# Optimization experiments

Hardware: AMD Instinct MI355X
Metric: run time of the kernel (lower is better)

## Reference

```python
import jax, jax.numpy as jnp
import numpy as np

V, B, T, D, F, E = 16000, 8, 1024, 64, 256, 8


def setup_inputs() -> dict:
    key = jax.random.key(0)
    ks = jax.random.split(key, 8)
    s = 0.02
    return {
        "x": jax.random.randint(ks[0], (B, T), 0, V),
        "embed_table": jax.random.normal(ks[1], (V, D), jnp.float32) * s,
        "Wm": jax.random.normal(ks[2], (D, D), jnp.float32) * s,
        "Um": jax.random.normal(ks[3], (D, D), jnp.float32) * s,
        "bm": jnp.zeros((D,), jnp.float32),
        "Wg": jax.random.normal(ks[4], (D, E), jnp.float32) * s,
        "bg": jnp.zeros((E,), jnp.float32),
        "W1": jax.random.normal(ks[5], (E, D, F), jnp.float32) * s,
        "b1": jnp.zeros((E, F), jnp.float32),
        "W2": jax.random.normal(ks[6], (E, F, D), jnp.float32) * s,
        "b2": jnp.zeros((E, D), jnp.float32),
        "ln_g": jnp.ones((D,), jnp.float32),
        "ln_b": jnp.zeros((D,), jnp.float32),
        "head_W": jax.random.normal(ks[7], (D, V), jnp.float32) * s,
        "head_b": jnp.zeros((V,), jnp.float32),
    }


def _layernorm(y, g, b, eps=1e-5):
    mu = jnp.mean(y, axis=-1, keepdims=True)
    var = jnp.mean((y - mu) ** 2, axis=-1, keepdims=True)
    return g * (y - mu) * jax.lax.rsqrt(var + eps) + b


def reference(x, embed_table, Wm, Um, bm, Wg, bg, W1, b1, W2, b2, ln_g, ln_b, head_W, head_b):
    emb = embed_table[x]                    # [B, T, D]
    emb_t = jnp.swapaxes(emb, 0, 1)         # [T, B, D] for scan over time

    def step(mem, x_t):
        # recurrent router: state update then gate computation
        mem_new = jnp.tanh(x_t @ Wm + mem @ Um + bm)              # [B, D]
        gates = jax.nn.softmax(mem_new @ Wg + bg, axis=-1)        # [B, E]
        # all-experts dense FFN (exact erf GELU as in torch default)
        h = jax.nn.gelu(jnp.einsum('bd,edf->bef', x_t, W1) + b1, approximate=False)
        eo = jnp.einsum('bef,efd->bed', h, W2) + b2               # [B, E, D]
        moe = jnp.einsum('be,bed->bd', gates, eo)                 # gated sum
        out_t = _layernorm(x_t + moe, ln_g, ln_b)
        return mem_new, out_t

    mem0 = jnp.zeros((x.shape[0], emb.shape[-1]), emb.dtype)
    _, outs = jax.lax.scan(step, mem0, emb_t)   # outs: [T, B, D]
    out = jnp.swapaxes(outs, 0, 1)              # [B, T, D]
    logits = out @ head_W + head_b              # [B, T, V]
    # training_mode=False -> no pred_loss branch; avg_pred_loss == 0.0
    return logits
```

## Files before the change

### kernel.cpp

```cpp
#include <hip/hip_runtime.h>


#define VV 16000
#define BB 8
#define TT 1024
#define DD 64
#define FF 256
#define EE 8
#define BT 8192

typedef unsigned short u16;
typedef unsigned int   u32;
typedef __attribute__((ext_vector_type(8))) short short8;
typedef __attribute__((ext_vector_type(4))) float f32x4;
typedef __attribute__((ext_vector_type(2))) float f32x2;

__device__ __forceinline__ float bf2f(u16 u) {
    union { u32 i; float f; } v; v.i = ((u32)u) << 16; return v.f;
}
__device__ __forceinline__ u16 f2bf(float f) {
    union { float f; u32 i; } v; v.f = f;
    u32 lsb = (v.i >> 16) & 1u;
    return (u16)((v.i + 0x7fffu + lsb) >> 16);
}
__device__ __forceinline__ short8 ld8(const u16* p) { return *(const short8*)p; }
__device__ __forceinline__ float ldf(const void* p, int i, int isbf) {
    return isbf ? bf2f(((const u16*)p)[i]) : ((const float*)p)[i];
}

__global__ __launch_bounds__(256) void k_sniff(const u32* __restrict__ tblw,
                                               int* __restrict__ flag) {
    __shared__ int c;
    int tid = threadIdx.x;
    if (tid == 0) c = 0;
    __syncthreads();
    u32 u = tblw[tid];
    u32 lo = u & 0xFFFFu;
    u32 e = (lo >> 7) & 0xFFu;
    int hit = ((e >= 0x60u && e <= 0x7Eu) || lo == 0u) ? 1 : 0;
    atomicAdd(&c, hit);
    __syncthreads();
    if (tid == 0) *flag = (c >= 192) ? 1 : 0;
}

__global__ __launch_bounds__(256) void k_transph(const void* __restrict__ headW,
                                                 const int* __restrict__ flag,
                                                 u16* __restrict__ headWT) {
    __shared__ float tile[DD][DD + 1];
    int isbf = *flag;
    int v0 = blockIdx.x * 64;
    int tid = threadIdx.x;
    int c = tid & 63, rq = tid >> 6;
#pragma unroll
    for (int i = 0; i < 16; i++) {
        int k = i * 4 + rq;
        tile[k][c] = ldf(headW, k * VV + v0 + c, isbf);
    }
    __syncthreads();
#pragma unroll
    for (int i = 0; i < 16; i++) {
        int v = i * 4 + rq;
        headWT[(v0 + v) * DD + c] = f2bf(tile[c][v]);
    }
}

__global__ __launch_bounds__(256) void k_transpose(const void* __restrict__ W1,
                                                   const void* __restrict__ W2,
                                                   const int* __restrict__ flag,
                                                   u16* __restrict__ W1T,
                                                   u16* __restrict__ W2T) {
    int isbf = *flag;
    int idx = blockIdx.x * 256 + threadIdx.x;
    if (idx < EE * DD * FF) {
        int e = idx >> 14, r = idx & 16383, d = r >> 8, f = r & 255;
        W1T[e * 16384 + f * DD + d] = f2bf(ldf(W1, idx, isbf));
    } else {
        int j2 = idx - EE * DD * FF;
        int e = j2 >> 14, r = j2 & 16383, f = r >> 6, d = r & 63;
        W2T[e * 16384 + d * FF + f] = f2bf(ldf(W2, j2, isbf));
    }
}

__global__ __launch_bounds__(256) void k_embed_pre(const int* __restrict__ x,
                                                   const void* __restrict__ tbl,
                                                   const void* __restrict__ Wm,
                                                   const void* __restrict__ bm,
                                                   const int* __restrict__ flag,
                                                   u16* __restrict__ emb,
                                                   float* __restrict__ pre) {
    __shared__ float sWm[DD * DD];
    __shared__ float sbm[DD];
    int isbf = *flag;
    int tid = threadIdx.x;
    for (int i = tid; i < DD * DD; i += 256) sWm[i] = ldf(Wm, i, isbf);
    if (tid < DD) sbm[tid] = ldf(bm, tid, isbf);
    __syncthreads();

    int gi = blockIdx.x * 256 + tid;
    int tok = gi >> 2, q = gi & 3;
    int id = x[tok];
    float e[DD];
    if (isbf) {
        const uint4* src = (const uint4*)((const u16*)tbl + id * DD);
        uint4* dst = (uint4*)(emb + tok * DD);
#pragma unroll
        for (int i = 0; i < 8; i++) {
            uint4 v = src[i];
            if ((i >> 1) == q) dst[i] = v;
            const u16* pu = (const u16*)&v;
#pragma unroll
            for (int j = 0; j < 8; j++) e[i * 8 + j] = bf2f(pu[j]);
        }
    } else {
        const float4* src = (const float4*)((const float*)tbl + id * DD);
        u16* dst = emb + tok * DD;
#pragma unroll
        for (int i = 0; i < 16; i++) {
            float4 v = src[i];
            e[i * 4 + 0] = v.x; e[i * 4 + 1] = v.y;
            e[i * 4 + 2] = v.z; e[i * 4 + 3] = v.w;
            if ((i >> 2) == q) {
                u32 p0 = (u32)f2bf(v.x) | ((u32)f2bf(v.y) << 16);
                u32 p1 = (u32)f2bf(v.z) | ((u32)f2bf(v.w) << 16);
                ((u32*)dst)[i * 2] = p0;
                ((u32*)dst)[i * 2 + 1] = p1;
            }
        }
    }
    int b = tok >> 10, t = tok & 1023;
    float* prow = pre + (t * BB + b) * DD + q * 16;
#pragma unroll
    for (int j4 = 0; j4 < 4; j4++) {
        int j0 = q * 16 + j4 * 4;
        float a0 = sbm[j0 + 0], a1 = sbm[j0 + 1];
        float a2 = sbm[j0 + 2], a3 = sbm[j0 + 3];
#pragma unroll
        for (int k = 0; k < DD; k++) {
            float ek = e[k];
            float4 wv = *(const float4*)&sWm[k * DD + j0];
            a0 += ek * wv.x; a1 += ek * wv.y;
            a2 += ek * wv.z; a3 += ek * wv.w;
        }
        ((float4*)prow)[j4] = make_float4(a0, a1, a2, a3);
    }
}

__global__ __launch_bounds__(64, 1) void k_scan(const float* __restrict__ pre,
                                                const void* __restrict__ Um,
                                                const int* __restrict__ flag,
                                                float* __restrict__ mem) {
    int isbf = *flag;
    int b = blockIdx.x, j = threadIdx.x;
    __shared__ float sm[DD];

    f32x2 c0, c1, c2, c3, c4, c5, c6, c7, c8, c9, c10, c11, c12, c13, c14, c15,
          c16, c17, c18, c19, c20, c21, c22, c23, c24, c25, c26, c27, c28, c29,
          c30, c31;
    if (isbf) {
        const u16* up = (const u16*)Um + j;
#define LDU(VAR, I) VAR = (f32x2){bf2f(up[(2 * I) * DD]), bf2f(up[(2 * I + 1) * DD])};
        LDU(c0, 0)  LDU(c1, 1)  LDU(c2, 2)  LDU(c3, 3)
        LDU(c4, 4)  LDU(c5, 5)  LDU(c6, 6)  LDU(c7, 7)
        LDU(c8, 8)  LDU(c9, 9)  LDU(c10, 10) LDU(c11, 11)
        LDU(c12, 12) LDU(c13, 13) LDU(c14, 14) LDU(c15, 15)
        LDU(c16, 16) LDU(c17, 17) LDU(c18, 18) LDU(c19, 19)
        LDU(c20, 20) LDU(c21, 21) LDU(c22, 22) LDU(c23, 23)
        LDU(c24, 24) LDU(c25, 25) LDU(c26, 26) LDU(c27, 27)
        LDU(c28, 28) LDU(c29, 29) LDU(c30, 30) LDU(c31, 31)
#undef LDU
    } else {
        const float* up = (const float*)Um + j;
#define LDU(VAR, I) VAR = (f32x2){up[(2 * I) * DD], up[(2 * I + 1) * DD]};
        LDU(c0, 0)  LDU(c1, 1)  LDU(c2, 2)  LDU(c3, 3)
        LDU(c4, 4)  LDU(c5, 5)  LDU(c6, 6)  LDU(c7, 7)
        LDU(c8, 8)  LDU(c9, 9)  LDU(c10, 10) LDU(c11, 11)
        LDU(c12, 12) LDU(c13, 13) LDU(c14, 14) LDU(c15, 15)
        LDU(c16, 16) LDU(c17, 17) LDU(c18, 18) LDU(c19, 19)
        LDU(c20, 20) LDU(c21, 21) LDU(c22, 22) LDU(c23, 23)
        LDU(c24, 24) LDU(c25, 25) LDU(c26, 26) LDU(c27, 27)
        LDU(c28, 28) LDU(c29, 29) LDU(c30, 30) LDU(c31, 31)
#undef LDU
    }
    sm[j] = 0.f;

    const float* pb = pre + b * DD + j;
    float* mbp = mem + b * DD + j;

    float p0 = pb[0 * 512], p1 = pb[1 * 512], p2 = pb[2 * 512], p3 = pb[3 * 512];
    float p4 = pb[4 * 512], p5 = pb[5 * 512], p6 = pb[6 * 512], p7 = pb[7 * 512];

    for (int c = 0; c < 128; ++c) {
        int nt0 = (c < 127) ? (c + 1) * 8 : 1016;
        const float* pn = pb + nt0 * 512;
        float q0 = pn[0 * 512], q1 = pn[1 * 512], q2 = pn[2 * 512], q3 = pn[3 * 512];
        float q4 = pn[4 * 512], q5 = pn[5 * 512], q6 = pn[6 * 512], q7 = pn[7 * 512];

        float m0, m1, m2, m3, m4r, m5, m6, m7;
#define STEP2(KK, UA, UB, UC, UD) {                             \
        f32x4 va = mv[2 * KK], vb = mv[2 * KK + 1];             \
        A0 += __builtin_shufflevector(va, va, 0, 1) * UA;       \
        A1 += __builtin_shufflevector(va, va, 2, 3) * UB;       \
        A2 += __builtin_shufflevector(vb, vb, 0, 1) * UC;       \
        A3 += __builtin_shufflevector(vb, vb, 2, 3) * UD; }
#define DOT_TANH(PIN, MOUT) {                                                  \
        const f32x4* mv = (const f32x4*)sm;                                    \
        f32x2 A0 = {0.f, 0.f}, A1 = {0.f, 0.f}, A2 = {0.f, 0.f}, A3 = {0.f, 0.f}; \
        STEP2(0, c0, c1, c2, c3)     STEP2(1, c4, c5, c6, c7)                  \
        STEP2(2, c8, c9, c10, c11)   STEP2(3, c12, c13, c14, c15)              \
        STEP2(4, c16, c17, c18, c19) STEP2(5, c20, c21, c22, c23)              \
        STEP2(6, c24, c25, c26, c27) STEP2(7, c28, c29, c30, c31)              \
        float s = ((A0.x + A0.y) + (A1.x + A1.y))                              \
                + ((A2.x + A2.y) + (A3.x + A3.y)) + PIN;                       \
        float ex = __expf(2.f * s);                                            \
        MOUT = 1.f - 2.f * __builtin_amdgcn_rcpf(ex + 1.f);                    \
        sm[j] = MOUT; }
        DOT_TANH(p0, m0) DOT_TANH(p1, m1) DOT_TANH(p2, m2) DOT_TANH(p3, m3)
        DOT_TANH(p4, m4r) DOT_TANH(p5, m5) DOT_TANH(p6, m6) DOT_TANH(p7, m7)
#undef DOT_TANH
#undef STEP2
        float* mp = mbp + c * 8 * 512;
        mp[0 * 512] = m0; mp[1 * 512] = m1; mp[2 * 512] = m2; mp[3 * 512] = m3;
        mp[4 * 512] = m4r; mp[5 * 512] = m5; mp[6 * 512] = m6; mp[7 * 512] = m7;
        p0 = q0; p1 = q1; p2 = q2; p3 = q3;
        p4 = q4; p5 = q5; p6 = q6; p7 = q7;
    }
}

__global__ __launch_bounds__(256) void k_ffn(const u16* __restrict__ emb,
                                             const u16* __restrict__ W1T,
                                             const void* __restrict__ b1g,
                                             const u16* __restrict__ W2T,
                                             const void* __restrict__ b2g,
                                             const int* __restrict__ flag,
                                             u16* __restrict__ eo) {
    __shared__ u16 hh[4][16 * 264];
    int isbf = *flag;
    int e = blockIdx.x, mb = blockIdx.y;
    int w = threadIdx.x >> 6, l = threadIdx.x & 63;
    int lr = l & 15, lq = l >> 4;
    int m0 = mb * 64 + w * 16;

    short8 a0 = ld8(emb + (m0 + lr) * DD + lq * 8);
    short8 a1 = ld8(emb + (m0 + lr) * DD + 32 + lq * 8);
    const u16* w1 = W1T + e * 16384;

    f32x4 acc[16];
#pragma unroll
    for (int nt = 0; nt < 16; nt++) {
        int n = nt * 16 + lr;
        short8 bf0 = ld8(w1 + n * DD + lq * 8);
        short8 bf1 = ld8(w1 + n * DD + 32 + lq * 8);
        f32x4 c = {0.f, 0.f, 0.f, 0.f};
        c = __builtin_amdgcn_mfma_f32_16x16x32_bf16(a0, bf0, c, 0, 0, 0);
        c = __builtin_amdgcn_mfma_f32_16x16x32_bf16(a1, bf1, c, 0, 0, 0);
        acc[nt] = c;
    }
    u16* hw = hh[w];
#pragma unroll
    for (int nt = 0; nt < 16; nt++) {
        int n = nt * 16 + lr;
        float bb = ldf(b1g, e * FF + n, isbf);
#pragma unroll
        for (int r = 0; r < 4; r++) {
            float xv = acc[nt][r] + bb;
            float g = 0.5f * xv * (1.f + erff(xv * 0.70710678118654752f));
            hw[(lq * 4 + r) * 264 + n] = f2bf(g);
        }
    }
    __syncthreads();

    f32x4 acc2[4];
#pragma unroll
    for (int dt = 0; dt < 4; dt++) acc2[dt] = (f32x4){0.f, 0.f, 0.f, 0.f};
    const u16* w2 = W2T + e * 16384;
#pragma unroll
    for (int kb = 0; kb < 8; kb++) {
        short8 af = ld8(hw + lr * 264 + kb * 32 + lq * 8);
#pragma unroll
        for (int dt = 0; dt < 4; dt++) {
            short8 bf = ld8(w2 + (dt * 16 + lr) * FF + kb * 32 + lq * 8);
            acc2[dt] = __builtin_amdgcn_mfma_f32_16x16x32_bf16(af, bf, acc2[dt], 0, 0, 0);
        }
    }
#pragma unroll
    for (int dt = 0; dt < 4; dt++) {
        int d = dt * 16 + lr;
        float bb = ldf(b2g, e * DD + d, isbf);
#pragma unroll
        for (int r = 0; r < 4; r++) {
            int tok = m0 + lq * 4 + r;
            eo[(tok * EE + e) * DD + d] = f2bf(acc2[dt][r] + bb);
        }
    }
}

__global__ __launch_bounds__(256) void k_gates(const float* __restrict__ mem,
                                               const void* __restrict__ Wg,
                                               const void* __restrict__ bg,
                                               const int* __restrict__ flag,
                                               float* __restrict__ gates) {
    __shared__ float sWg[DD * EE];
    int isbf = *flag;
    int tid = threadIdx.x;
    for (int i = tid; i < DD * EE; i += 256) sWg[i] = ldf(Wg, i, isbf);
    __syncthreads();

    int tok = blockIdx.x * 256 + tid;
    int b = tok >> 10, t = tok & 1023;
    const float* mr = mem + (t * BB + b) * DD;
    float z[EE];
#pragma unroll
    for (int e = 0; e < EE; e++) z[e] = ldf(bg, e, isbf);
    const float4* wg4 = (const float4*)sWg;
    const float4* mr4 = (const float4*)mr;
    for (int k4 = 0; k4 < 16; k4++) {
        float4 mv = mr4[k4];
        float m[4] = {mv.x, mv.y, mv.z, mv.w};
#pragma unroll
        for (int kk = 0; kk < 4; kk++) {
            int k = k4 * 4 + kk;
            float4 wa = wg4[k * 2], wb = wg4[k * 2 + 1];
            z[0] += m[kk] * wa.x; z[1] += m[kk] * wa.y;
            z[2] += m[kk] * wa.z; z[3] += m[kk] * wa.w;
            z[4] += m[kk] * wb.x; z[5] += m[kk] * wb.y;
            z[6] += m[kk] * wb.z; z[7] += m[kk] * wb.w;
        }
    }
    float zm = z[0];
#pragma unroll
    for (int e = 1; e < EE; e++) zm = fmaxf(zm, z[e]);
    float sum = 0.f;
#pragma unroll
    for (int e = 0; e < EE; e++) { z[e] = __expf(z[e] - zm); sum += z[e]; }
    float rs = __builtin_amdgcn_rcpf(sum);
#pragma unroll
    for (int e = 0; e < EE; e++) gates[tok * EE + e] = z[e] * rs;
}

__global__ __launch_bounds__(256) void k_ln(const u16* __restrict__ emb,
                                            const u16* __restrict__ eo,
                                            const float* __restrict__ gates,
                                            const void* __restrict__ ln_g,
                                            const void* __restrict__ ln_b,
                                            const int* __restrict__ flag,
                                            u16* __restrict__ outb) {
    int isbf = *flag;
    int w = threadIdx.x >> 6, l = threadIdx.x & 63;
    int tok = blockIdx.x * 4 + w;
    const float* g = gates + tok * EE;
    const u16* er = eo + tok * EE * DD;
    float moe = 0.f;
#pragma unroll
    for (int e = 0; e < EE; e++) moe += g[e] * bf2f(er[e * DD + l]);
    float y = bf2f(emb[tok * DD + l]) + moe;
    float s = y;
#pragma unroll
    for (int off = 32; off > 0; off >>= 1) s += __shfl_xor(s, off, 64);
    float mu = s * (1.f / 64.f);
    float d = y - mu;
    float s2 = d * d;
#pragma unroll
    for (int off = 32; off > 0; off >>= 1) s2 += __shfl_xor(s2, off, 64);
    float var = s2 * (1.f / 64.f);
    float r = rsqrtf(var + 1e-5f);
    float o = ldf(ln_g, l, isbf) * d * r + ldf(ln_b, l, isbf);
    outb[tok * DD + l] = f2bf(o);
}

__global__ __launch_bounds__(256) void k_head(const u16* __restrict__ outb,
                                              const u16* __restrict__ headWT,
                                              const void* __restrict__ head_b,
                                              const int* __restrict__ flag,
                                              void* __restrict__ logits) {
    int isbf = *flag;
    int nb = blockIdx.x, mb = blockIdx.y;
    int w = threadIdx.x >> 6, l = threadIdx.x & 63;
    int lr = l & 15, lq = l >> 4;
    int m0 = mb * 64 + w * 16;
    int n0 = nb * 256;
    int ntc = (nb == 62) ? 8 : 16;

    short8 a0 = ld8(outb + (m0 + lr) * DD + lq * 8);
    short8 a1 = ld8(outb + (m0 + lr) * DD + 32 + lq * 8);

    for (int nt = 0; nt < ntc; nt++) {
        int n = n0 + nt * 16 + lr;
        short8 bf0 = ld8(headWT + n * DD + lq * 8);
        short8 bf1 = ld8(headWT + n * DD + 32 + lq * 8);
        f32x4 c = {0.f, 0.f, 0.f, 0.f};
        c = __builtin_amdgcn_mfma_f32_16x16x32_bf16(a0, bf0, c, 0, 0, 0);
        c = __builtin_amdgcn_mfma_f32_16x16x32_bf16(a1, bf1, c, 0, 0, 0);
        float hb = ldf(head_b, n, isbf);
        if (isbf) {
#pragma unroll
            for (int r = 0; r < 4; r++)
                ((u16*)logits)[(m0 + lq * 4 + r) * VV + n] = f2bf(c[r] + hb);
        } else {
#pragma unroll
            for (int r = 0; r < 4; r++)
                ((float*)logits)[(m0 + lq * 4 + r) * VV + n] = c[r] + hb;
        }
    }
}

extern "C" void kernel_launch(void* const* d_in, const int* in_sizes, int n_in,
                              void* d_out, int out_size, void* d_ws, size_t ws_size,
                              hipStream_t stream) {
    const int*  x      = (const int*)d_in[0];
    const void* tbl    = d_in[1];
    const void* Wm     = d_in[2];
    const void* Um     = d_in[3];
    const void* bm     = d_in[4];
    const void* Wg     = d_in[5];
    const void* bg     = d_in[6];
    const void* W1     = d_in[7];
    const void* b1     = d_in[8];
    const void* W2     = d_in[9];
    const void* b2     = d_in[10];
    const void* ln_g   = d_in[11];
    const void* ln_b   = d_in[12];
    const void* headW  = d_in[13];
    const void* head_b = d_in[14];

    char* w = (char*)d_ws;
    int*   flag   = (int*)(w);
    u16*   headWT = (u16*)(w + 0x0000100);
    u16*   W1T    = (u16*)(w + 0x0200000);
    u16*   W2T    = (u16*)(w + 0x0240000);
    u16*   emb    = (u16*)(w + 0x0280000);
    u16*   outb   = (u16*)(w + 0x0380000);
    float* pre    = (float*)(w + 0x0480000);
    float* mem    = (float*)(w + 0x0680000);
    float* gates  = (float*)(w + 0x0880000);
    u16*   eo     = (u16*)(w + 0x08C0000);

    k_sniff<<<dim3(1), dim3(256), 0, stream>>>((const u32*)tbl, flag);
    k_transph<<<dim3(VV / 64), dim3(256), 0, stream>>>(headW, flag, headWT);
    k_transpose<<<dim3(2 * EE * DD * FF / 256), dim3(256), 0, stream>>>(
        W1, W2, flag, W1T, W2T);
    k_embed_pre<<<dim3(BT * 4 / 256), dim3(256), 0, stream>>>(x, tbl, Wm, bm, flag, emb, pre);
    k_scan<<<dim3(BB), dim3(64), 0, stream>>>(pre, Um, flag, mem);
    k_ffn<<<dim3(EE, BT / 64), dim3(256), 0, stream>>>(emb, W1T, b1, W2T, b2, flag, eo);
    k_gates<<<dim3(BT / 256), dim3(256), 0, stream>>>(mem, Wg, bg, flag, gates);
    k_ln<<<dim3(BT / 4), dim3(256), 0, stream>>>(emb, eo, gates, ln_g, ln_b, flag, outb);
    k_head<<<dim3(63, BT / 64), dim3(256), 0, stream>>>(outb, headWT, head_b, flag, d_out);
}
```

Before: 1.109 ms.

## Fuse serial scan and expert FFN into one launch to overlap them

Measured after the change: 975.0 us. 1.14x faster.

```diff
diff --git a/kernel.cpp b/kernel.cpp
--- a/kernel.cpp
+++ b/kernel.cpp
@@ -145,97 +145,90 @@
     }
 }
 
-__global__ __launch_bounds__(64, 1) void k_scan(const float* __restrict__ pre,
-                                                const void* __restrict__ Um,
-                                                const int* __restrict__ flag,
-                                                float* __restrict__ mem) {
-    int isbf = *flag;
-    int b = blockIdx.x, j = threadIdx.x;
-    __shared__ float sm[DD];
-
-    f32x2 c0, c1, c2, c3, c4, c5, c6, c7, c8, c9, c10, c11, c12, c13, c14, c15,
-          c16, c17, c18, c19, c20, c21, c22, c23, c24, c25, c26, c27, c28, c29,
-          c30, c31;
-    if (isbf) {
-        const u16* up = (const u16*)Um + j;
+__global__ __launch_bounds__(256, 1) void k_scan_ffn(
+        const float* __restrict__ pre, const void* __restrict__ Um,
+        const u16* __restrict__ emb, const u16* __restrict__ W1T,
+        const void* __restrict__ b1g, const u16* __restrict__ W2T,
+        const void* __restrict__ b2g, const int* __restrict__ flag,
+        float* __restrict__ mem, u16* __restrict__ eo) {
+    __shared__ u16 hh[4][16 * 264];
+    int isbf = *flag;
+    int bid = blockIdx.x;
+
+    if (bid < BB) {
+        if (threadIdx.x >= 64) return;
+        int b = bid, j = threadIdx.x;
+        float* sm = (float*)hh;
+
+        f32x2 c0, c1, c2, c3, c4, c5, c6, c7, c8, c9, c10, c11, c12, c13,
+              c14, c15, c16, c17, c18, c19, c20, c21, c22, c23, c24, c25,
+              c26, c27, c28, c29, c30, c31;
+        if (isbf) {
+            const u16* up = (const u16*)Um + j;
 #define LDU(VAR, I) VAR = (f32x2){bf2f(up[(2 * I) * DD]), bf2f(up[(2 * I + 1) * DD])};
-        LDU(c0, 0)  LDU(c1, 1)  LDU(c2, 2)  LDU(c3, 3)
-        LDU(c4, 4)  LDU(c5, 5)  LDU(c6, 6)  LDU(c7, 7)
-        LDU(c8, 8)  LDU(c9, 9)  LDU(c10, 10) LDU(c11, 11)
-        LDU(c12, 12) LDU(c13, 13) LDU(c14, 14) LDU(c15, 15)
-        LDU(c16, 16) LDU(c17, 17) LDU(c18, 18) LDU(c19, 19)
-        LDU(c20, 20) LDU(c21, 21) LDU(c22, 22) LDU(c23, 23)
-        LDU(c24, 24) LDU(c25, 25) LDU(c26, 26) LDU(c27, 27)
-        LDU(c28, 28) LDU(c29, 29) LDU(c30, 30) LDU(c31, 31)
+            LDU(c0, 0)  LDU(c1, 1)  LDU(c2, 2)  LDU(c3, 3)
+            LDU(c4, 4)  LDU(c5, 5)  LDU(c6, 6)  LDU(c7, 7)
+            LDU(c8, 8)  LDU(c9, 9)  LDU(c10, 10) LDU(c11, 11)
+            LDU(c12, 12) LDU(c13, 13) LDU(c14, 14) LDU(c15, 15)
+            LDU(c16, 16) LDU(c17, 17) LDU(c18, 18) LDU(c19, 19)
+            LDU(c20, 20) LDU(c21, 21) LDU(c22, 22) LDU(c23, 23)
+            LDU(c24, 24) LDU(c25, 25) LDU(c26, 26) LDU(c27, 27)
+            LDU(c28, 28) LDU(c29, 29) LDU(c30, 30) LDU(c31, 31)
 #undef LDU
-    } else {
-        const float* up = (const float*)Um + j;
+        } else {
+            const float* up = (const float*)Um + j;
 #define LDU(VAR, I) VAR = (f32x2){up[(2 * I) * DD], up[(2 * I + 1) * DD]};
-        LDU(c0, 0)  LDU(c1, 1)  LDU(c2, 2)  LDU(c3, 3)
-        LDU(c4, 4)  LDU(c5, 5)  LDU(c6, 6)  LDU(c7, 7)
-        LDU(c8, 8)  LDU(c9, 9)  LDU(c10, 10) LDU(c11, 11)
-        LDU(c12, 12) LDU(c13, 13) LDU(c14, 14) LDU(c15, 15)
-        LDU(c16, 16) LDU(c17, 17) LDU(c18, 18) LDU(c19, 19)
-        LDU(c20, 20) LDU(c21, 21) LDU(c22, 22) LDU(c23, 23)
-        LDU(c24, 24) LDU(c25, 25) LDU(c26, 26) LDU(c27, 27)
-        LDU(c28, 28) LDU(c29, 29) LDU(c30, 30) LDU(c31, 31)
+            LDU(c0, 0)  LDU(c1, 1)  LDU(c2, 2)  LDU(c3, 3)
+            LDU(c4, 4)  LDU(c5, 5)  LDU(c6, 6)  LDU(c7, 7)
+            LDU(c8, 8)  LDU(c9, 9)  LDU(c10, 10) LDU(c11, 11)
+            LDU(c12, 12) LDU(c13, 13) LDU(c14, 14) LDU(c15, 15)
+            LDU(c16, 16) LDU(c17, 17) LDU(c18, 18) LDU(c19, 19)
+            LDU(c20, 20) LDU(c21, 21) LDU(c22, 22) LDU(c23, 23)
+            LDU(c24, 24) LDU(c25, 25) LDU(c26, 26) LDU(c27, 27)
+            LDU(c28, 28) LDU(c29, 29) LDU(c30, 30) LDU(c31, 31)
 #undef LDU
-    }
-    sm[j] = 0.f;
-
-    const float* pb = pre + b * DD + j;
-    float* mbp = mem + b * DD + j;
-
-    float p0 = pb[0 * 512], p1 = pb[1 * 512], p2 = pb[2 * 512], p3 = pb[3 * 512];
-    float p4 = pb[4 * 512], p5 = pb[5 * 512], p6 = pb[6 * 512], p7 = pb[7 * 512];
-
-    for (int c = 0; c < 128; ++c) {
-        int nt0 = (c < 127) ? (c + 1) * 8 : 1016;
-        const float* pn = pb + nt0 * 512;
-        float q0 = pn[0 * 512], q1 = pn[1 * 512], q2 = pn[2 * 512], q3 = pn[3 * 512];
-        float q4 = pn[4 * 512], q5 = pn[5 * 512], q6 = pn[6 * 512], q7 = pn[7 * 512];
-
-        float m0, m1, m2, m3, m4r, m5, m6, m7;
+        }
+        asm volatile("" : "+v"(c0), "+v"(c1), "+v"(c2), "+v"(c3),
+                          "+v"(c4), "+v"(c5), "+v"(c6), "+v"(c7));
+        asm volatile("" : "+v"(c8), "+v"(c9), "+v"(c10), "+v"(c11),
+                          "+v"(c12), "+v"(c13), "+v"(c14), "+v"(c15));
+        asm volatile("" : "+v"(c16), "+v"(c17), "+v"(c18), "+v"(c19),
+                          "+v"(c20), "+v"(c21), "+v"(c22), "+v"(c23));
+        asm volatile("" : "+v"(c24), "+v"(c25), "+v"(c26), "+v"(c27),
+                          "+v"(c28), "+v"(c29), "+v"(c30), "+v"(c31));
+        sm[j] = 0.f;
+
+        float pcur = pre[b * DD + j];
+        for (int t = 0; t < TT; t++) {
+            int tn = (t + 1 < TT) ? t + 1 : t;
+            float pnext = pre[(tn * BB + b) * DD + j];
+            const f32x4* mv = (const f32x4*)sm;
+            f32x2 A0 = {0.f, 0.f}, A1 = {0.f, 0.f};
+            f32x2 A2 = {0.f, 0.f}, A3 = {0.f, 0.f};
 #define STEP2(KK, UA, UB, UC, UD) {                             \
-        f32x4 va = mv[2 * KK], vb = mv[2 * KK + 1];             \
-        A0 += __builtin_shufflevector(va, va, 0, 1) * UA;       \
-        A1 += __builtin_shufflevector(va, va, 2, 3) * UB;       \
-        A2 += __builtin_shufflevector(vb, vb, 0, 1) * UC;       \
-        A3 += __builtin_shufflevector(vb, vb, 2, 3) * UD; }
-#define DOT_TANH(PIN, MOUT) {                                                  \
-        const f32x4* mv = (const f32x4*)sm;                                    \
-        f32x2 A0 = {0.f, 0.f}, A1 = {0.f, 0.f}, A2 = {0.f, 0.f}, A3 = {0.f, 0.f}; \
-        STEP2(0, c0, c1, c2, c3)     STEP2(1, c4, c5, c6, c7)                  \
-        STEP2(2, c8, c9, c10, c11)   STEP2(3, c12, c13, c14, c15)              \
-        STEP2(4, c16, c17, c18, c19) STEP2(5, c20, c21, c22, c23)              \
-        STEP2(6, c24, c25, c26, c27) STEP2(7, c28, c29, c30, c31)              \
-        float s = ((A0.x + A0.y) + (A1.x + A1.y))                              \
-                + ((A2.x + A2.y) + (A3.x + A3.y)) + PIN;                       \
-        float ex = __expf(2.f * s);                                            \
-        MOUT = 1.f - 2.f * __builtin_amdgcn_rcpf(ex + 1.f);                    \
-        sm[j] = MOUT; }
-        DOT_TANH(p0, m0) DOT_TANH(p1, m1) DOT_TANH(p2, m2) DOT_TANH(p3, m3)
-        DOT_TANH(p4, m4r) DOT_TANH(p5, m5) DOT_TANH(p6, m6) DOT_TANH(p7, m7)
-#undef DOT_TANH
+            f32x4 va = mv[2 * KK], vb = mv[2 * KK + 1];         \
+            A0 += __builtin_shufflevector(va, va, 0, 1) * UA;   \
+            A1 += __builtin_shufflevector(va, va, 2, 3) * UB;   \
+            A2 += __builtin_shufflevector(vb, vb, 0, 1) * UC;   \
+            A3 += __builtin_shufflevector(vb, vb, 2, 3) * UD; }
+            STEP2(0, c0, c1, c2, c3)     STEP2(1, c4, c5, c6, c7)
+            STEP2(2, c8, c9, c10, c11)   STEP2(3, c12, c13, c14, c15)
+            STEP2(4, c16, c17, c18, c19) STEP2(5, c20, c21, c22, c23)
+            STEP2(6, c24, c25, c26, c27) STEP2(7, c28, c29, c30, c31)
 #undef STEP2
-        float* mp = mbp + c * 8 * 512;
-        mp[0 * 512] = m0; mp[1 * 512] = m1; mp[2 * 512] = m2; mp[3 * 512] = m3;
-        mp[4 * 512] = m4r; mp[5 * 512] = m5; mp[6 * 512] = m6; mp[7 * 512] = m7;
-        p0 = q0; p1 = q1; p2 = q2; p3 = q3;
-        p4 = q4; p5 = q5; p6 = q6; p7 = q7;
-    }
-}
-
-__global__ __launch_bounds__(256) void k_ffn(const u16* __restrict__ emb,
-                                             const u16* __restrict__ W1T,
-                                             const void* __restrict__ b1g,
-                                             const u16* __restrict__ W2T,
-                                             const void* __restrict__ b2g,
-                                             const int* __restrict__ flag,
-                                             u16* __restrict__ eo) {
-    __shared__ u16 hh[4][16 * 264];
-    int isbf = *flag;
-    int e = blockIdx.x, mb = blockIdx.y;
+            float s = ((A0.x + A0.y) + (A1.x + A1.y))
+                    + ((A2.x + A2.y) + (A3.x + A3.y)) + pcur;
+            float ex = __expf(2.f * s);
+            float mn = 1.f - 2.f * __builtin_amdgcn_rcpf(ex + 1.f);
+            sm[j] = mn;
+            mem[(t * BB + b) * DD + j] = mn;
+            pcur = pnext;
+        }
+        return;
+    }
+
+    int fid = bid - BB;
+    int e = fid >> 7, mb = fid & 127;
     int w = threadIdx.x >> 6, l = threadIdx.x & 63;
     int lr = l & 15, lq = l >> 4;
     int m0 = mb * 64 + w * 16;
@@ -439,8 +432,8 @@
     k_transpose<<<dim3(2 * EE * DD * FF / 256), dim3(256), 0, stream>>>(
         W1, W2, flag, W1T, W2T);
     k_embed_pre<<<dim3(BT * 4 / 256), dim3(256), 0, stream>>>(x, tbl, Wm, bm, flag, emb, pre);
-    k_scan<<<dim3(BB), dim3(64), 0, stream>>>(pre, Um, flag, mem);
-    k_ffn<<<dim3(EE, BT / 64), dim3(256), 0, stream>>>(emb, W1T, b1, W2T, b2, flag, eo);
+    k_scan_ffn<<<dim3(BB + EE * (BT / 64)), dim3(256), 0, stream>>>(
+        pre, Um, emb, W1T, b1, W2T, b2, flag, mem, eo);
     k_gates<<<dim3(BT / 256), dim3(256), 0, stream>>>(mem, Wg, bg, flag, gates);
     k_ln<<<dim3(BT / 4), dim3(256), 0, stream>>>(emb, eo, gates, ln_g, ln_b, flag, outb);
     k_head<<<dim3(63, BT / 64), dim3(256), 0, stream>>>(outb, headWT, head_b, flag, d_out);
```
